# Performance work log

Hardware: AMD Instinct MI355X
Metric: run time of the kernel (lower is better)

The kernel has to match this reference:

```python
import jax, jax.numpy as jnp
import numpy as np

T, B = 64, 8  # rollout steps x envs; x rows = T*B


def _conv2d(x, w, b=None, pad=1):
    y = jax.lax.conv_general_dilated(x, w, (1, 1), [(pad, pad), (pad, pad)],
                                     dimension_numbers=("NCHW", "OIHW", "NCHW"))
    return y if b is None else y + b[None, :, None, None]


def _maxpool3s2(x):
    return jax.lax.reduce_window(x, -jnp.inf, jax.lax.max, (1, 1, 3, 3), (1, 1, 2, 2),
                                 [(0, 0), (0, 0), (1, 1), (1, 1)])


def _conv_seq(x, cw, cb, rw, rb):
    # Conv -> MaxPool -> ResBlock -> ResBlock
    x = _maxpool3s2(_conv2d(x, cw, cb))
    for i in range(2):
        o = jax.nn.relu(x)
        o = _conv2d(o, rw[2 * i], rb[2 * i])
        o = jax.nn.relu(o)
        o = _conv2d(o, rw[2 * i + 1], rb[2 * i + 1])
        x = o + x
    return x


def _cbam(x, fc1, fc2, spw):
    mlp = lambda v: jax.nn.relu(v @ fc1.T) @ fc2.T
    ca = jax.nn.sigmoid(mlp(x.mean((2, 3))) + mlp(x.max((2, 3))))  # channel attention
    x = x * ca[:, :, None, None]
    sp = jnp.concatenate([x.mean(1, keepdims=True), x.max(1, keepdims=True)], axis=1)
    sa = jax.nn.sigmoid(_conv2d(sp, spw, None, pad=3))  # 7x7 spatial attention
    return x * sa


def setup_inputs():
    key = jax.random.key(0)
    ks = iter(jax.random.split(key, 40))
    f = lambda shape, s=0.05: jax.random.normal(next(ks), shape, jnp.float32) * s
    return {
        "x": f((T * B, 6, 128, 128), 1.0),
        "done": jnp.zeros((T * B,), jnp.float32),
        "gru_state": f((1, B, 128), 1.0),
        "s0_cw": f((16, 6, 3, 3)), "s0_cb": jnp.zeros((16,), jnp.float32),
        "s0_rw": f((4, 16, 16, 3, 3)), "s0_rb": jnp.zeros((4, 16), jnp.float32),
        "s1_cw": f((32, 16, 3, 3)), "s1_cb": jnp.zeros((32,), jnp.float32),
        "s1_rw": f((4, 32, 32, 3, 3)), "s1_rb": jnp.zeros((4, 32), jnp.float32),
        "s2_cw": f((32, 32, 3, 3)), "s2_cb": jnp.zeros((32,), jnp.float32),
        "s2_rw": f((4, 32, 32, 3, 3)), "s2_rb": jnp.zeros((4, 32), jnp.float32),
        "cbam_fc1": f((8, 32)), "cbam_fc2": f((32, 8)), "cbam_spw": f((1, 2, 7, 7)),
        "fc_w": f((256, 8192), 0.01), "fc_b": jnp.zeros((256,), jnp.float32),
        "gru_wih": f((384, 256)), "gru_whh": f((384, 128)),
        "gru_bih": jnp.zeros((384,), jnp.float32), "gru_bhh": jnp.zeros((384,), jnp.float32),
        "actor_w": f((3, 128), 0.01), "actor_b": jnp.zeros((3,), jnp.float32),
        "critic_w": f((1, 128)), "critic_b": jnp.zeros((1,), jnp.float32),
    }


def reference(x, done, gru_state,
              s0_cw, s0_cb, s0_rw, s0_rb,
              s1_cw, s1_cb, s1_rw, s1_rb,
              s2_cw, s2_cb, s2_rw, s2_rb,
              cbam_fc1, cbam_fc2, cbam_spw,
              fc_w, fc_b, gru_wih, gru_whh, gru_bih, gru_bhh,
              actor_w, actor_b, critic_w, critic_b):
    h = _conv_seq(x, s0_cw, s0_cb, s0_rw, s0_rb)  # (TB,16,64,64)
    h = _conv_seq(h, s1_cw, s1_cb, s1_rw, s1_rb)  # (TB,32,32,32)
    h = _conv_seq(h, s2_cw, s2_cb, s2_rw, s2_rb)  # (TB,32,16,16)
    h = jax.nn.relu(h)
    h = _cbam(h, cbam_fc1, cbam_fc2, cbam_spw)
    feat = jax.nn.relu(h.reshape(h.shape[0], -1) @ fc_w.T + fc_b)  # (TB,256)
    seq = feat.reshape(T, B, 256)
    d = done.reshape(T, B)
    h0 = gru_state[0]  # (B,128)

    def step(hprev, xd):
        xt, dt = xd
        hprev = (1.0 - dt)[:, None] * hprev  # done-masking of recurrent state
        gi = xt @ gru_wih.T + gru_bih
        gh = hprev @ gru_whh.T + gru_bhh
        ir, iz, inn = jnp.split(gi, 3, axis=-1)
        hr, hz, hn = jnp.split(gh, 3, axis=-1)
        r = jax.nn.sigmoid(ir + hr)
        z = jax.nn.sigmoid(iz + hz)
        n = jnp.tanh(inn + r * hn)
        hnew = (1.0 - z) * n + z * hprev
        return hnew, hnew

    _, hs = jax.lax.scan(step, h0, (seq, d))  # hs: (T,B,128)
    hidden = hs.reshape(T * B, 128)
    logits = hidden @ actor_w.T + actor_b
    value = hidden @ critic_w.T + critic_b
    return jnp.concatenate([logits, value], axis=-1)  # (TB, n_actions+1)
```

## Files before the change

### kernel.cpp

```cpp
#include <hip/hip_runtime.h>
#include <cstdint>
#include <cfloat>
#include <cmath>

typedef unsigned short ushort_t;
typedef short bf16x8 __attribute__((ext_vector_type(8)));
typedef float f32x4 __attribute__((ext_vector_type(4)));

__device__ inline ushort_t f2bf(float f) {
    union { float f; unsigned u; } v; v.f = f;
    return (ushort_t)((v.u + 0x7fffu + ((v.u >> 16) & 1u)) >> 16);
}
__device__ inline float bf2f(ushort_t u) {
    union { unsigned u; float f; } v; v.u = ((unsigned)u) << 16;
    return v.f;
}
__device__ inline float bflo_f(unsigned w) { union { unsigned u; float f; } v; v.u = w << 16; return v.f; }
__device__ inline float bfhi_f(unsigned w) { union { unsigned u; float f; } v; v.u = w & 0xFFFF0000u; return v.f; }
__device__ inline unsigned pk2(float a, float b) {
    return (unsigned)f2bf(a) | ((unsigned)f2bf(b) << 16);
}
__device__ inline unsigned relu2(unsigned p) {
    unsigned lo = (p & 0x8000u) ? 0u : (p & 0xFFFFu);
    unsigned hi = (p & 0x80000000u) ? 0u : (p & 0xFFFF0000u);
    return lo | hi;
}

struct PPJob { const float* src; ushort_t* dst; int ci; int co; };
struct PPArgs { PPJob j[15]; };

__global__ __launch_bounds__(256) void prepack_k(PPArgs a) {
    const PPJob p = a.j[blockIdx.x];
    const int tot = 9 * p.co * 32;
    for (int i = threadIdx.x; i < tot; i += 256) {
        const int cip = i & 31;
        const int rest = i >> 5;
        const int co = rest % p.co;
        const int pos = rest / p.co;
        float v = 0.f;
        if (cip < p.ci) v = p.src[(co * p.ci + cip) * 9 + pos];
        p.dst[i] = f2bf(v);
    }
}

template<int CIR, int CO, bool NCHWIN>
__global__ __launch_bounds__(256) void convm_k(
    const void* __restrict__ inv, const ushort_t* __restrict__ wp,
    const float* __restrict__ bias, const ushort_t* __restrict__ skip,
    ushort_t* __restrict__ out, int H, int TX, int relu_in)
{
    constexpr int NT = CO / 16;
    __shared__ __align__(16) ushort_t in_t[18 * 18 * 40];

    const int n    = blockIdx.y;
    const int tile = blockIdx.x;
    const int ty0  = (tile / TX) * 16, tx0 = (tile % TX) * 16;
    const int tid  = threadIdx.x;
    const int lane = tid & 63, wv = tid >> 6;
    const int col  = lane & 15, oct = lane >> 4;

    bf16x8 wfrag[9][NT];
    #pragma unroll
    for (int p = 0; p < 9; ++p)
        #pragma unroll
        for (int t = 0; t < NT; ++t)
            wfrag[p][t] = *(const bf16x8*)&wp[(p * CO + t * 16 + col) * 32 + oct * 8];

    if constexpr (NCHWIN) {
        for (int i = tid; i < 18 * 18 * 40 / 8; i += 256)
            *(uint4*)&in_t[i * 8] = make_uint4(0, 0, 0, 0);
        __syncthreads();
        const float* gin = (const float*)inv;
        for (int i = tid; i < CIR * 324; i += 256) {
            const int ci = i / 324, px = i % 324;
            const int r = px / 18, c = px % 18;
            const int gy = ty0 - 1 + r, gx = tx0 - 1 + c;
            if ((unsigned)gy < (unsigned)H && (unsigned)gx < (unsigned)H)
                in_t[px * 40 + ci] = f2bf(gin[(((size_t)n * CIR + ci) * H + gy) * H + gx]);
        }
    } else {
        const ushort_t* gin = (const ushort_t*)inv;
        for (int i = tid; i < 324 * 4; i += 256) {
            const int px = i >> 2, oc = i & 3;
            const int r = px / 18, c = px % 18;
            const int gy = ty0 - 1 + r, gx = tx0 - 1 + c;
            uint4 v = make_uint4(0, 0, 0, 0);
            if (oc * 8 < CIR && (unsigned)gy < (unsigned)H && (unsigned)gx < (unsigned)H) {
                v = *(const uint4*)&gin[(((size_t)n * H + gy) * H + gx) * CIR + oc * 8];
                if (relu_in) { v.x = relu2(v.x); v.y = relu2(v.y); v.z = relu2(v.z); v.w = relu2(v.w); }
            }
            *(uint4*)&in_t[px * 40 + oc * 8] = v;
        }
    }
    __syncthreads();

    f32x4 acc[4][NT];
    #pragma unroll
    for (int r = 0; r < 4; ++r)
        #pragma unroll
        for (int t = 0; t < NT; ++t)
            acc[r][t] = (f32x4){0.f, 0.f, 0.f, 0.f};

    #pragma unroll
    for (int p = 0; p < 9; ++p) {
        const int ky = p / 3, kx = p % 3;
        #pragma unroll
        for (int r = 0; r < 4; ++r) {
            const int iy = wv * 4 + r + ky;
            const int ix = col + kx;
            const bf16x8 b = *(const bf16x8*)&in_t[(iy * 18 + ix) * 40 + oct * 8];
            #pragma unroll
            for (int t = 0; t < NT; ++t)
                acc[r][t] = __builtin_amdgcn_mfma_f32_16x16x32_bf16(wfrag[p][t], b, acc[r][t], 0, 0, 0);
        }
    }

    float4 bv[NT];
    #pragma unroll
    for (int t = 0; t < NT; ++t) bv[t] = *(const float4*)&bias[t * 16 + oct * 4];
    #pragma unroll
    for (int r = 0; r < 4; ++r) {
        const int gy = ty0 + wv * 4 + r;
        const int gx = tx0 + col;
        const size_t pbase = (((size_t)n * H + gy) * H + gx) * CO + oct * 4;
        #pragma unroll
        for (int t = 0; t < NT; ++t) {
            float v0 = acc[r][t][0] + bv[t].x;
            float v1 = acc[r][t][1] + bv[t].y;
            float v2 = acc[r][t][2] + bv[t].z;
            float v3 = acc[r][t][3] + bv[t].w;
            if (skip) {
                const uint2 s = *(const uint2*)&skip[pbase + t * 16];
                v0 += bflo_f(s.x); v1 += bfhi_f(s.x);
                v2 += bflo_f(s.y); v3 += bfhi_f(s.y);
            }
            uint2 o;
            o.x = pk2(v0, v1);
            o.y = pk2(v2, v3);
            *(uint2*)&out[pbase + t * 16] = o;
        }
    }
}

__global__ __launch_bounds__(256) void pool_nhwc_k(
    const ushort_t* __restrict__ in, ushort_t* __restrict__ out,
    int NI, int H, int C)
{
    const int HP = H >> 1, C8 = C >> 3;
    const long total = (long)NI * HP * HP * C8;
    long idx = (long)blockIdx.x * 256 + threadIdx.x;
    if (idx >= total) return;
    const int c8 = (int)(idx % C8); long r = idx / C8;
    const int px = (int)(r % HP); r /= HP;
    const int py = (int)(r % HP); const long n = r / HP;
    float m[8];
    #pragma unroll
    for (int k = 0; k < 8; ++k) m[k] = -FLT_MAX;
    for (int dy = 0; dy < 3; ++dy) {
        const int y = 2 * py - 1 + dy;
        if ((unsigned)y >= (unsigned)H) continue;
        for (int dx = 0; dx < 3; ++dx) {
            const int x = 2 * px - 1 + dx;
            if ((unsigned)x >= (unsigned)H) continue;
            const uint4 v = *(const uint4*)&in[(((long)n * H + y) * H + x) * C + c8 * 8];
            m[0] = fmaxf(m[0], bflo_f(v.x)); m[1] = fmaxf(m[1], bfhi_f(v.x));
            m[2] = fmaxf(m[2], bflo_f(v.y)); m[3] = fmaxf(m[3], bfhi_f(v.y));
            m[4] = fmaxf(m[4], bflo_f(v.z)); m[5] = fmaxf(m[5], bfhi_f(v.z));
            m[6] = fmaxf(m[6], bflo_f(v.w)); m[7] = fmaxf(m[7], bfhi_f(v.w));
        }
    }
    uint4 o;
    o.x = (unsigned)f2bf(m[0]) | ((unsigned)f2bf(m[1]) << 16);
    o.y = (unsigned)f2bf(m[2]) | ((unsigned)f2bf(m[3]) << 16);
    o.z = (unsigned)f2bf(m[4]) | ((unsigned)f2bf(m[5]) << 16);
    o.w = (unsigned)f2bf(m[6]) | ((unsigned)f2bf(m[7]) << 16);
    *(uint4*)&out[(((long)n * HP + py) * HP + px) * C + c8 * 8] = o;
}

__global__ __launch_bounds__(256) void gemm_splitk_k(
    const float* __restrict__ A, const float* __restrict__ B,
    float* __restrict__ partial, int M, int N, int K, int KC)
{
    __shared__ __align__(16) float As[32][65];
    __shared__ __align__(16) float Bs[32][65];
    const int m0 = blockIdx.x * 64, n0 = blockIdx.y * 64;
    const int kbase = blockIdx.z * KC;
    const int tid = threadIdx.x;
    const int tx = tid & 15, ty = tid >> 4;

    float acc[4][4];
    #pragma unroll
    for (int i = 0; i < 4; ++i)
        #pragma unroll
        for (int j = 0; j < 4; ++j) acc[i][j] = 0.f;

    for (int k0 = kbase; k0 < kbase + KC; k0 += 32) {
        for (int i = tid; i < 64 * 32; i += 256) {
            const int m = i >> 5, k = i & 31;
            As[k][m] = A[(size_t)(m0 + m) * K + k0 + k];
        }
        for (int i = tid; i < 64 * 32; i += 256) {
            const int nn = i >> 5, k = i & 31;
            Bs[k][nn] = B[(size_t)(n0 + nn) * K + k0 + k];
        }
        __syncthreads();
        #pragma unroll
        for (int k = 0; k < 32; ++k) {
            const float4 a = *(const float4*)&As[k][ty * 4];
            const float4 b = *(const float4*)&Bs[k][tx * 4];
            acc[0][0] = fmaf(a.x, b.x, acc[0][0]);
            acc[0][1] = fmaf(a.x, b.y, acc[0][1]);
            acc[0][2] = fmaf(a.x, b.z, acc[0][2]);
            acc[0][3] = fmaf(a.x, b.w, acc[0][3]);
            acc[1][0] = fmaf(a.y, b.x, acc[1][0]);
            acc[1][1] = fmaf(a.y, b.y, acc[1][1]);
            acc[1][2] = fmaf(a.y, b.z, acc[1][2]);
            acc[1][3] = fmaf(a.y, b.w, acc[1][3]);
            acc[2][0] = fmaf(a.z, b.x, acc[2][0]);
            acc[2][1] = fmaf(a.z, b.y, acc[2][1]);
            acc[2][2] = fmaf(a.z, b.z, acc[2][2]);
            acc[2][3] = fmaf(a.z, b.w, acc[2][3]);
            acc[3][0] = fmaf(a.w, b.x, acc[3][0]);
            acc[3][1] = fmaf(a.w, b.y, acc[3][1]);
            acc[3][2] = fmaf(a.w, b.z, acc[3][2]);
            acc[3][3] = fmaf(a.w, b.w, acc[3][3]);
        }
        __syncthreads();
    }

    float* pbase = partial + (size_t)blockIdx.z * M * N;
    #pragma unroll
    for (int i = 0; i < 4; ++i) {
        float4 o = make_float4(acc[i][0], acc[i][1], acc[i][2], acc[i][3]);
        *(float4*)&pbase[(size_t)(m0 + ty * 4 + i) * N + n0 + tx * 4] = o;
    }
}

__global__ __launch_bounds__(256) void gemm_reduce_k(
    const float* __restrict__ partial, const float* __restrict__ bias,
    float* __restrict__ out, int MN, int N, int S, int relu)
{
    const int idx = blockIdx.x * 256 + threadIdx.x;
    if (idx >= MN) return;
    float s = bias[idx % N];
    for (int i = 0; i < S; ++i) s += partial[(size_t)i * MN + idx];
    if (relu) s = fmaxf(s, 0.f);
    out[idx] = s;
}

__global__ __launch_bounds__(256) void cbam_k(
    const ushort_t* __restrict__ in, const float* __restrict__ fc1,
    const float* __restrict__ fc2, const float* __restrict__ spw,
    float* __restrict__ out)
{
    __shared__ float xl[32][257];
    __shared__ float cmean[32], cmax[32], hidm[8], hidx[8], ca[32];
    __shared__ float spm[256], spx[256], sa[256];
    const int n = blockIdx.x, tid = threadIdx.x;
    const ushort_t* inN = in + (size_t)n * 8192;
    #pragma unroll
    for (int c8 = 0; c8 < 4; ++c8) {
        const uint4 v = *(const uint4*)&inN[tid * 32 + c8 * 8];
        xl[c8 * 8 + 0][tid] = fmaxf(bflo_f(v.x), 0.f);
        xl[c8 * 8 + 1][tid] = fmaxf(bfhi_f(v.x), 0.f);
        xl[c8 * 8 + 2][tid] = fmaxf(bflo_f(v.y), 0.f);
        xl[c8 * 8 + 3][tid] = fmaxf(bfhi_f(v.y), 0.f);
        xl[c8 * 8 + 4][tid] = fmaxf(bflo_f(v.z), 0.f);
        xl[c8 * 8 + 5][tid] = fmaxf(bfhi_f(v.z), 0.f);
        xl[c8 * 8 + 6][tid] = fmaxf(bflo_f(v.w), 0.f);
        xl[c8 * 8 + 7][tid] = fmaxf(bfhi_f(v.w), 0.f);
    }
    __syncthreads();
    if (tid < 32) {
        float s = 0.f, m = -FLT_MAX;
        for (int p = 0; p < 256; ++p) { float v = xl[tid][p]; s += v; m = fmaxf(m, v); }
        cmean[tid] = s * (1.f / 256.f); cmax[tid] = m;
    }
    __syncthreads();
    if (tid < 8) {
        float sm = 0.f, sx = 0.f;
        for (int c = 0; c < 32; ++c) {
            float f = fc1[tid * 32 + c];
            sm += f * cmean[c]; sx += f * cmax[c];
        }
        hidm[tid] = fmaxf(sm, 0.f); hidx[tid] = fmaxf(sx, 0.f);
    }
    __syncthreads();
    if (tid < 32) {
        float s = 0.f;
        for (int h = 0; h < 8; ++h) s += fc2[tid * 8 + h] * (hidm[h] + hidx[h]);
        ca[tid] = 1.f / (1.f + expf(-s));
    }
    __syncthreads();
    {
        float s = 0.f, m = -FLT_MAX;
        for (int c = 0; c < 32; ++c) {
            float v = xl[c][tid] * ca[c];
            xl[c][tid] = v;
            s += v; m = fmaxf(m, v);
        }
        spm[tid] = s * (1.f / 32.f); spx[tid] = m;
    }
    __syncthreads();
    {
        const int y = tid >> 4, x = tid & 15;
        float s = 0.f;
        for (int ky = 0; ky < 7; ++ky) {
            const int yy = y + ky - 3;
            if (yy < 0 || yy >= 16) continue;
            for (int kx = 0; kx < 7; ++kx) {
                const int xx = x + kx - 3;
                if (xx < 0 || xx >= 16) continue;
                const int p = yy * 16 + xx;
                s += spm[p] * spw[ky * 7 + kx] + spx[p] * spw[49 + ky * 7 + kx];
            }
        }
        sa[tid] = 1.f / (1.f + expf(-s));
    }
    __syncthreads();
    float* outN = out + (size_t)n * 8192;
    const float sav = sa[tid];
    for (int c = 0; c < 32; ++c) outN[c * 256 + tid] = xl[c][tid] * sav;
}

__global__ __launch_bounds__(384) void gru_k(
    const float* __restrict__ gi, const float* __restrict__ done,
    const float* __restrict__ h0, const float* __restrict__ whh,
    const float* __restrict__ bhh, float* __restrict__ hidden)
{
    const int b = blockIdx.x, j = threadIdx.x;
    __shared__ __align__(16) float hl[128];
    __shared__ float gh[384];
    float4 wr[32];
    const float4* wrow = (const float4*)(whh + (size_t)j * 128);
    #pragma unroll
    for (int i = 0; i < 32; ++i) wr[i] = wrow[i];
    const float bj = bhh[j];
    if (j < 128) hl[j] = h0[b * 128 + j];
    __syncthreads();
    for (int t = 0; t < 64; ++t) {
        const int rowi = t * 8 + b;
        const float dmask = 1.f - done[rowi];
        if (j < 128) hl[j] *= dmask;
        __syncthreads();
        float s = bj;
        const float4* h4 = (const float4*)hl;
        #pragma unroll
        for (int i = 0; i < 32; ++i) {
            const float4 h = h4[i];
            s = fmaf(wr[i].x, h.x, s);
            s = fmaf(wr[i].y, h.y, s);
            s = fmaf(wr[i].z, h.z, s);
            s = fmaf(wr[i].w, h.w, s);
        }
        gh[j] = s;
        __syncthreads();
        if (j < 128) {
            const float* gir = gi + (size_t)rowi * 384;
            const float r = 1.f / (1.f + expf(-(gir[j] + gh[j])));
            const float z = 1.f / (1.f + expf(-(gir[128 + j] + gh[128 + j])));
            const float nn = tanhf(gir[256 + j] + r * gh[256 + j]);
            const float hm = hl[j];
            const float hn = (1.f - z) * nn + z * hm;
            hl[j] = hn;
            hidden[(size_t)rowi * 128 + j] = hn;
        }
        __syncthreads();
    }
}

__global__ __launch_bounds__(256) void heads_k(
    const float* __restrict__ hidden, const float* __restrict__ aw,
    const float* __restrict__ ab, const float* __restrict__ cw,
    const float* __restrict__ cb, float* __restrict__ out)
{
    const int idx = blockIdx.x * 256 + threadIdx.x;
    const int m = idx >> 2, c = idx & 3;
    const float* h = hidden + (size_t)m * 128;
    const float* w = (c < 3) ? (aw + (size_t)c * 128) : cw;
    float s = (c < 3) ? ab[c] : cb[0];
    for (int k = 0; k < 128; ++k) s = fmaf(h[k], w[k], s);
    out[idx] = s;
}

extern "C" void kernel_launch(void* const* d_in, const int* in_sizes, int n_in,
                              void* d_out, int out_size, void* d_ws, size_t ws_size,
                              hipStream_t stream)
{
    const float* x      = (const float*)d_in[0];
    const float* done   = (const float*)d_in[1];
    const float* gstate = (const float*)d_in[2];
    const float* s0_cw  = (const float*)d_in[3];
    const float* s0_cb  = (const float*)d_in[4];
    const float* s0_rw  = (const float*)d_in[5];
    const float* s0_rb  = (const float*)d_in[6];
    const float* s1_cw  = (const float*)d_in[7];
    const float* s1_cb  = (const float*)d_in[8];
    const float* s1_rw  = (const float*)d_in[9];
    const float* s1_rb  = (const float*)d_in[10];
    const float* s2_cw  = (const float*)d_in[11];
    const float* s2_cb  = (const float*)d_in[12];
    const float* s2_rw  = (const float*)d_in[13];
    const float* s2_rb  = (const float*)d_in[14];
    const float* cfc1   = (const float*)d_in[15];
    const float* cfc2   = (const float*)d_in[16];
    const float* cspw   = (const float*)d_in[17];
    const float* fc_w   = (const float*)d_in[18];
    const float* fc_b   = (const float*)d_in[19];
    const float* gwih   = (const float*)d_in[20];
    const float* gwhh   = (const float*)d_in[21];
    const float* gbih   = (const float*)d_in[22];
    const float* gbhh   = (const float*)d_in[23];
    const float* aw     = (const float*)d_in[24];
    const float* ab     = (const float*)d_in[25];
    const float* cwt    = (const float*)d_in[26];
    const float* cbs    = (const float*)d_in[27];
    float* out = (float*)d_out;

    ushort_t* wsu = (ushort_t*)d_ws;
    ushort_t* SCR = wsu;
    ushort_t* U1  = wsu + 33554432;
    ushort_t* U3  = wsu + 67108864;
    ushort_t* X0  = wsu + 83886080;
    ushort_t* WP  = wsu + 88080384;
    float* CBO   = (float*)SCR;
    float* PART  = (float*)U1;
    float* FEAT  = PART + 4194304;
    float* GI    = FEAT + 131072;
    float* PARTG = GI + 196608;
    float* HID   = PARTG + 786432;

    ushort_t* wp_s0e = WP;
    ushort_t* wp_s0r = WP + 4608;
    ushort_t* wp_s1e = WP + 23040;
    ushort_t* wp_s1r = WP + 32256;
    ushort_t* wp_s2e = WP + 69120;
    ushort_t* wp_s2r = WP + 78336;
    {
        PPArgs a;
        a.j[0] = {s0_cw, wp_s0e, 6, 16};
        for (int i = 0; i < 4; ++i) a.j[1 + i] = {s0_rw + i * 2304, wp_s0r + i * 4608, 16, 16};
        a.j[5] = {s1_cw, wp_s1e, 16, 32};
        for (int i = 0; i < 4; ++i) a.j[6 + i] = {s1_rw + i * 9216, wp_s1r + i * 9216, 32, 32};
        a.j[10] = {s2_cw, wp_s2e, 32, 32};
        for (int i = 0; i < 4; ++i) a.j[11 + i] = {s2_rw + i * 9216, wp_s2r + i * 9216, 32, 32};
        prepack_k<<<15, 256, 0, stream>>>(a);
    }

    for (int c = 0; c < 4; ++c) {
        const float* xin = x + (size_t)c * 128 * 6 * 128 * 128;
        convm_k<6, 16, true><<<dim3(64, 128), 256, 0, stream>>>(
            xin, wp_s0e, s0_cb, nullptr, SCR, 128, 8, 0);
        pool_nhwc_k<<<4096, 256, 0, stream>>>(SCR, U1 + (size_t)c * 8388608, 128, 128, 16);
    }
    convm_k<16, 16, false><<<dim3(16, 512), 256, 0, stream>>>(U1,  wp_s0r + 0 * 4608, s0_rb + 0,  nullptr, SCR, 64, 4, 1);
    convm_k<16, 16, false><<<dim3(16, 512), 256, 0, stream>>>(SCR, wp_s0r + 1 * 4608, s0_rb + 16, U1,      U1,  64, 4, 1);
    convm_k<16, 16, false><<<dim3(16, 512), 256, 0, stream>>>(U1,  wp_s0r + 2 * 4608, s0_rb + 32, nullptr, SCR, 64, 4, 1);
    convm_k<16, 16, false><<<dim3(16, 512), 256, 0, stream>>>(SCR, wp_s0r + 3 * 4608, s0_rb + 48, U1,      U1,  64, 4, 1);
    for (int c = 0; c < 2; ++c) {
        convm_k<16, 32, false><<<dim3(16, 256), 256, 0, stream>>>(
            U1 + (size_t)c * 16777216, wp_s1e, s1_cb, nullptr, SCR, 64, 4, 0);
        pool_nhwc_k<<<4096, 256, 0, stream>>>(SCR, U3 + (size_t)c * 8388608, 256, 64, 32);
    }
    convm_k<32, 32, false><<<dim3(4, 512), 256, 0, stream>>>(U3,  wp_s1r + 0 * 9216, s1_rb + 0,  nullptr, SCR, 32, 2, 1);
    convm_k<32, 32, false><<<dim3(4, 512), 256, 0, stream>>>(SCR, wp_s1r + 1 * 9216, s1_rb + 32, U3,      U3,  32, 2, 1);
    convm_k<32, 32, false><<<dim3(4, 512), 256, 0, stream>>>(U3,  wp_s1r + 2 * 9216, s1_rb + 64, nullptr, SCR, 32, 2, 1);
    convm_k<32, 32, false><<<dim3(4, 512), 256, 0, stream>>>(SCR, wp_s1r + 3 * 9216, s1_rb + 96, U3,      U3,  32, 2, 1);
    convm_k<32, 32, false><<<dim3(4, 512), 256, 0, stream>>>(U3, wp_s2e, s2_cb, nullptr, SCR, 32, 2, 0);
    pool_nhwc_k<<<2048, 256, 0, stream>>>(SCR, X0, 512, 32, 32);
    convm_k<32, 32, false><<<dim3(1, 512), 256, 0, stream>>>(X0,  wp_s2r + 0 * 9216, s2_rb + 0,  nullptr, SCR, 16, 1, 1);
    convm_k<32, 32, false><<<dim3(1, 512), 256, 0, stream>>>(SCR, wp_s2r + 1 * 9216, s2_rb + 32, X0,      X0,  16, 1, 1);
    convm_k<32, 32, false><<<dim3(1, 512), 256, 0, stream>>>(X0,  wp_s2r + 2 * 9216, s2_rb + 64, nullptr, SCR, 16, 1, 1);
    convm_k<32, 32, false><<<dim3(1, 512), 256, 0, stream>>>(SCR, wp_s2r + 3 * 9216, s2_rb + 96, X0,      X0,  16, 1, 1);
    cbam_k<<<512, 256, 0, stream>>>(X0, cfc1, cfc2, cspw, CBO);
    gemm_splitk_k<<<dim3(8, 4, 32), 256, 0, stream>>>(CBO, fc_w, PART, 512, 256, 8192, 256);
    gemm_reduce_k<<<512, 256, 0, stream>>>(PART, fc_b, FEAT, 512 * 256, 256, 32, 1);
    gemm_splitk_k<<<dim3(8, 6, 4), 256, 0, stream>>>(FEAT, gwih, PARTG, 512, 384, 256, 64);
    gemm_reduce_k<<<768, 256, 0, stream>>>(PARTG, gbih, GI, 512 * 384, 384, 4, 0);
    gru_k<<<8, 384, 0, stream>>>(GI, done, gstate, gwhh, gbhh, HID);
    heads_k<<<8, 256, 0, stream>>>(HID, aw, ab, cwt, cbs, out);
}
```

Baseline: 1.318 ms.

## Pack multiple kernel taps into the MFMA K dimension for low-channel convs

Repacks the conv weights so that the 32-wide K dimension of each bf16 MFMA holds several horizontal kernel taps when there are fewer than 32 input channels. CI=6 packs all 3 kx taps into one MFMA and CI=16 packs two taps, cutting the MFMA count from 9 to 3 or 6 per output tile where K was previously zero-padded. The input tile is staged with only the needed channel octets, the first layer loads channel pairs packed together, and B fragments are reused across ky rows. The cost is more complex shared-memory indexing, an extra padding row, and a different packed weight layout with new offsets.

```diff
diff --git a/kernel.cpp b/kernel.cpp
--- a/kernel.cpp
+++ b/kernel.cpp
@@ -26,19 +26,26 @@
     return lo | hi;
 }
 
-struct PPJob { const float* src; ushort_t* dst; int ci; int co; };
+struct PPJob { const float* src; ushort_t* dst; int ci; int co; int ci8; };
 struct PPArgs { PPJob j[15]; };
 
 __global__ __launch_bounds__(256) void prepack_k(PPArgs a) {
     const PPJob p = a.j[blockIdx.x];
-    const int tot = 9 * p.co * 32;
+    const int G  = (p.ci8 == 1) ? 1 : (p.ci8 == 2) ? 2 : 3;
+    const int cw = p.ci8 * 8;
+    const int S  = 4 / p.ci8;
+    const int tot = 3 * G * p.co * 32;
     for (int i = threadIdx.x; i < tot; i += 256) {
-        const int cip = i & 31;
+        const int k = i & 31;
         const int rest = i >> 5;
         const int co = rest % p.co;
-        const int pos = rest / p.co;
+        const int rest2 = rest / p.co;
+        const int g = rest2 % G;
+        const int ky = rest2 / G;
+        const int s = k / cw, cio = k % cw;
+        const int kx = g * S + s;
         float v = 0.f;
-        if (cip < p.ci) v = p.src[(co * p.ci + cip) * 9 + pos];
+        if (kx < 3 && cio < p.ci) v = p.src[(co * p.ci + cio) * 9 + ky * 3 + kx];
         p.dst[i] = f2bf(v);
     }
 }
@@ -49,8 +56,10 @@
     const float* __restrict__ bias, const ushort_t* __restrict__ skip,
     ushort_t* __restrict__ out, int H, int TX, int relu_in)
 {
-    constexpr int NT = CO / 16;
-    __shared__ __align__(16) ushort_t in_t[18 * 18 * 40];
+    constexpr int NT  = CO / 16;
+    constexpr int CI8 = (CIR + 7) / 8;
+    constexpr int G   = (CI8 == 1) ? 1 : (CI8 == 2) ? 2 : 3;
+    __shared__ __align__(16) ushort_t in_t[18 * 18 * 40 + 64];
 
     const int n    = blockIdx.y;
     const int tile = blockIdx.x;
@@ -59,33 +68,41 @@
     const int lane = tid & 63, wv = tid >> 6;
     const int col  = lane & 15, oct = lane >> 4;
 
-    bf16x8 wfrag[9][NT];
-    #pragma unroll
-    for (int p = 0; p < 9; ++p)
-        #pragma unroll
-        for (int t = 0; t < NT; ++t)
-            wfrag[p][t] = *(const bf16x8*)&wp[(p * CO + t * 16 + col) * 32 + oct * 8];
+    bf16x8 wfrag[3][G][NT];
+    #pragma unroll
+    for (int ky = 0; ky < 3; ++ky)
+        #pragma unroll
+        for (int g = 0; g < G; ++g)
+            #pragma unroll
+            for (int t = 0; t < NT; ++t)
+                wfrag[ky][g][t] = *(const bf16x8*)&wp[(((ky * G + g) * CO) + t * 16 + col) * 32 + oct * 8];
 
     if constexpr (NCHWIN) {
-        for (int i = tid; i < 18 * 18 * 40 / 8; i += 256)
-            *(uint4*)&in_t[i * 8] = make_uint4(0, 0, 0, 0);
+        for (int i = tid; i < 325; i += 256)
+            *(uint4*)&in_t[i * 40] = make_uint4(0, 0, 0, 0);
         __syncthreads();
         const float* gin = (const float*)inv;
-        for (int i = tid; i < CIR * 324; i += 256) {
-            const int ci = i / 324, px = i % 324;
+        constexpr int PR = (CIR + 1) / 2;
+        for (int i = tid; i < PR * 324; i += 256) {
+            const int px = i % 324, pr = i / 324;
             const int r = px / 18, c = px % 18;
             const int gy = ty0 - 1 + r, gx = tx0 - 1 + c;
-            if ((unsigned)gy < (unsigned)H && (unsigned)gx < (unsigned)H)
-                in_t[px * 40 + ci] = f2bf(gin[(((size_t)n * CIR + ci) * H + gy) * H + gx]);
+            if ((unsigned)gy < (unsigned)H && (unsigned)gx < (unsigned)H) {
+                const size_t b0 = (((size_t)n * CIR + pr * 2) * H + gy) * H + gx;
+                const float va = gin[b0];
+                const float vb = (pr * 2 + 1 < CIR) ? gin[b0 + (size_t)H * H] : 0.f;
+                *(unsigned*)&in_t[px * 40 + pr * 2] = pk2(va, vb);
+            }
         }
     } else {
+        if (tid < 4) *(uint4*)&in_t[324 * 40 + tid * 8] = make_uint4(0, 0, 0, 0);
         const ushort_t* gin = (const ushort_t*)inv;
-        for (int i = tid; i < 324 * 4; i += 256) {
-            const int px = i >> 2, oc = i & 3;
+        for (int i = tid; i < 324 * CI8; i += 256) {
+            const int px = i / CI8, oc = i % CI8;
             const int r = px / 18, c = px % 18;
             const int gy = ty0 - 1 + r, gx = tx0 - 1 + c;
             uint4 v = make_uint4(0, 0, 0, 0);
-            if (oc * 8 < CIR && (unsigned)gy < (unsigned)H && (unsigned)gx < (unsigned)H) {
+            if ((unsigned)gy < (unsigned)H && (unsigned)gx < (unsigned)H) {
                 v = *(const uint4*)&gin[(((size_t)n * H + gy) * H + gx) * CIR + oc * 8];
                 if (relu_in) { v.x = relu2(v.x); v.y = relu2(v.y); v.z = relu2(v.z); v.w = relu2(v.w); }
             }
@@ -101,23 +118,49 @@
         for (int t = 0; t < NT; ++t)
             acc[r][t] = (f32x4){0.f, 0.f, 0.f, 0.f};
 
-    #pragma unroll
-    for (int p = 0; p < 9; ++p) {
-        const int ky = p / 3, kx = p % 3;
-        #pragma unroll
-        for (int r = 0; r < 4; ++r) {
-            const int iy = wv * 4 + r + ky;
-            const int ix = col + kx;
-            const bf16x8 b = *(const bf16x8*)&in_t[(iy * 18 + ix) * 40 + oct * 8];
+    if constexpr (CI8 <= 2) {
+        bf16x8 bv[6][G];
+        #pragma unroll
+        for (int q = 0; q < 6; ++q) {
+            const int iy = wv * 4 + q;
             #pragma unroll
-            for (int t = 0; t < NT; ++t)
-                acc[r][t] = __builtin_amdgcn_mfma_f32_16x16x32_bf16(wfrag[p][t], b, acc[r][t], 0, 0, 0);
-        }
-    }
-
-    float4 bv[NT];
-    #pragma unroll
-    for (int t = 0; t < NT; ++t) bv[t] = *(const float4*)&bias[t * 16 + oct * 4];
+            for (int g = 0; g < G; ++g) {
+                int pix, cho;
+                if constexpr (CI8 == 1) { pix = col + oct;                 cho = 0; }
+                else                    { pix = col + g * 2 + (oct >> 1);  cho = (oct & 1) * 8; }
+                bv[q][g] = *(const bf16x8*)&in_t[(iy * 18 + pix) * 40 + cho];
+            }
+        }
+        #pragma unroll
+        for (int ky = 0; ky < 3; ++ky)
+            #pragma unroll
+            for (int r = 0; r < 4; ++r)
+                #pragma unroll
+                for (int g = 0; g < G; ++g)
+                    #pragma unroll
+                    for (int t = 0; t < NT; ++t)
+                        acc[r][t] = __builtin_amdgcn_mfma_f32_16x16x32_bf16(
+                            wfrag[ky][g][t], bv[r + ky][g], acc[r][t], 0, 0, 0);
+    } else {
+        #pragma unroll
+        for (int ky = 0; ky < 3; ++ky)
+            #pragma unroll
+            for (int r = 0; r < 4; ++r) {
+                const int iy = wv * 4 + r + ky;
+                #pragma unroll
+                for (int g = 0; g < 3; ++g) {
+                    const bf16x8 b = *(const bf16x8*)&in_t[(iy * 18 + col + g) * 40 + oct * 8];
+                    #pragma unroll
+                    for (int t = 0; t < NT; ++t)
+                        acc[r][t] = __builtin_amdgcn_mfma_f32_16x16x32_bf16(
+                            wfrag[ky][g][t], b, acc[r][t], 0, 0, 0);
+                }
+            }
+    }
+
+    float4 bv4[NT];
+    #pragma unroll
+    for (int t = 0; t < NT; ++t) bv4[t] = *(const float4*)&bias[t * 16 + oct * 4];
     #pragma unroll
     for (int r = 0; r < 4; ++r) {
         const int gy = ty0 + wv * 4 + r;
@@ -125,10 +168,10 @@
         const size_t pbase = (((size_t)n * H + gy) * H + gx) * CO + oct * 4;
         #pragma unroll
         for (int t = 0; t < NT; ++t) {
-            float v0 = acc[r][t][0] + bv[t].x;
-            float v1 = acc[r][t][1] + bv[t].y;
-            float v2 = acc[r][t][2] + bv[t].z;
-            float v3 = acc[r][t][3] + bv[t].w;
+            float v0 = acc[r][t][0] + bv4[t].x;
+            float v1 = acc[r][t][1] + bv4[t].y;
+            float v2 = acc[r][t][2] + bv4[t].z;
+            float v3 = acc[r][t][3] + bv4[t].w;
             if (skip) {
                 const uint2 s = *(const uint2*)&skip[pbase + t * 16];
                 v0 += bflo_f(s.x); v1 += bfhi_f(s.x);
@@ -431,19 +474,19 @@
     float* HID   = PARTG + 786432;
 
     ushort_t* wp_s0e = WP;
-    ushort_t* wp_s0r = WP + 4608;
-    ushort_t* wp_s1e = WP + 23040;
-    ushort_t* wp_s1r = WP + 32256;
-    ushort_t* wp_s2e = WP + 69120;
-    ushort_t* wp_s2r = WP + 78336;
+    ushort_t* wp_s0r = WP + 1536;
+    ushort_t* wp_s1e = WP + 13824;
+    ushort_t* wp_s1r = WP + 19968;
+    ushort_t* wp_s2e = WP + 56832;
+    ushort_t* wp_s2r = WP + 66048;
     {
         PPArgs a;
-        a.j[0] = {s0_cw, wp_s0e, 6, 16};
-        for (int i = 0; i < 4; ++i) a.j[1 + i] = {s0_rw + i * 2304, wp_s0r + i * 4608, 16, 16};
-        a.j[5] = {s1_cw, wp_s1e, 16, 32};
-        for (int i = 0; i < 4; ++i) a.j[6 + i] = {s1_rw + i * 9216, wp_s1r + i * 9216, 32, 32};
-        a.j[10] = {s2_cw, wp_s2e, 32, 32};
-        for (int i = 0; i < 4; ++i) a.j[11 + i] = {s2_rw + i * 9216, wp_s2r + i * 9216, 32, 32};
+        a.j[0] = {s0_cw, wp_s0e, 6, 16, 1};
+        for (int i = 0; i < 4; ++i) a.j[1 + i] = {s0_rw + i * 2304, wp_s0r + i * 3072, 16, 16, 2};
+        a.j[5] = {s1_cw, wp_s1e, 16, 32, 2};
+        for (int i = 0; i < 4; ++i) a.j[6 + i] = {s1_rw + i * 9216, wp_s1r + i * 9216, 32, 32, 4};
+        a.j[10] = {s2_cw, wp_s2e, 32, 32, 4};
+        for (int i = 0; i < 4; ++i) a.j[11 + i] = {s2_rw + i * 9216, wp_s2r + i * 9216, 32, 32, 4};
         prepack_k<<<15, 256, 0, stream>>>(a);
     }
 
@@ -453,10 +496,10 @@
             xin, wp_s0e, s0_cb, nullptr, SCR, 128, 8, 0);
         pool_nhwc_k<<<4096, 256, 0, stream>>>(SCR, U1 + (size_t)c * 8388608, 128, 128, 16);
     }
-    convm_k<16, 16, false><<<dim3(16, 512), 256, 0, stream>>>(U1,  wp_s0r + 0 * 4608, s0_rb + 0,  nullptr, SCR, 64, 4, 1);
-    convm_k<16, 16, false><<<dim3(16, 512), 256, 0, stream>>>(SCR, wp_s0r + 1 * 4608, s0_rb + 16, U1,      U1,  64, 4, 1);
-    convm_k<16, 16, false><<<dim3(16, 512), 256, 0, stream>>>(U1,  wp_s0r + 2 * 4608, s0_rb + 32, nullptr, SCR, 64, 4, 1);
-    convm_k<16, 16, false><<<dim3(16, 512), 256, 0, stream>>>(SCR, wp_s0r + 3 * 4608, s0_rb + 48, U1,      U1,  64, 4, 1);
+    convm_k<16, 16, false><<<dim3(16, 512), 256, 0, stream>>>(U1,  wp_s0r + 0 * 3072, s0_rb + 0,  nullptr, SCR, 64, 4, 1);
+    convm_k<16, 16, false><<<dim3(16, 512), 256, 0, stream>>>(SCR, wp_s0r + 1 * 3072, s0_rb + 16, U1,      U1,  64, 4, 1);
+    convm_k<16, 16, false><<<dim3(16, 512), 256, 0, stream>>>(U1,  wp_s0r + 2 * 3072, s0_rb + 32, nullptr, SCR, 64, 4, 1);
+    convm_k<16, 16, false><<<dim3(16, 512), 256, 0, stream>>>(SCR, wp_s0r + 3 * 3072, s0_rb + 48, U1,      U1,  64, 4, 1);
     for (int c = 0; c < 2; ++c) {
         convm_k<16, 32, false><<<dim3(16, 256), 256, 0, stream>>>(
             U1 + (size_t)c * 16777216, wp_s1e, s1_cb, nullptr, SCR, 64, 4, 0);
```

Result: faster. 1.143 ms (-13.3%).
